# Kernel tuning notes

Measured on AMD Instinct MI355X. Metric: run time of the kernel, lower is better.

The kernel has to match this reference:

```python
import jax, jax.numpy as jnp
import numpy as np

K = 16
EPS = 1e-5  # BatchNorm eps (torch default)


def _lin(t, w, b):
    # 1x1 Conv2d over channel dim == per-point linear
    return jnp.einsum('bnkc,cd->bnkd', t, w) + b


def _bn(t, g, b):
    # BatchNorm2d (training-mode batch stats) over all dims except channels
    m = jnp.mean(t, axis=(0, 1, 2), keepdims=True)
    v = jnp.var(t, axis=(0, 1, 2), keepdims=True)
    return (t - m) * jax.lax.rsqrt(v + EPS) * g + b


def setup_inputs() -> dict:
    key = jax.random.key(0)
    ks = jax.random.split(key, 8)
    B, N, C, OUT = 4, 4096, 61, 128
    IN = C + 3  # 64 = in_feat_dim

    def w(k, i, o):
        return jax.random.normal(k, (i, o), jnp.float32) * (1.0 / np.sqrt(i))

    return {
        'x': jax.random.normal(ks[0], (B, N, C), jnp.float32),
        'pos': jax.random.uniform(ks[1], (B, N, 3), jnp.float32),
        # relation_vec_to_weights_net: 10 -> 32 -> IN -> IN (no BN, last_act=False)
        'rw1': w(ks[2], 10, 32), 'rb1': jnp.zeros((32,), jnp.float32),
        'rw2': w(ks[3], 32, IN), 'rb2': jnp.zeros((IN,), jnp.float32),
        'rw3': w(ks[4], IN, IN), 'rb3': jnp.zeros((IN,), jnp.float32),
        # feat_mlp_net: IN -> OUT -> OUT (BN, last_act=False)
        'fw1': w(ks[5], IN, OUT), 'fb1': jnp.zeros((OUT,), jnp.float32),
        'g1': jnp.ones((OUT,), jnp.float32), 'b1': jnp.zeros((OUT,), jnp.float32),
        'fw2': w(ks[6], OUT, OUT), 'fb2': jnp.zeros((OUT,), jnp.float32),
        'g2': jnp.ones((OUT,), jnp.float32), 'b2': jnp.zeros((OUT,), jnp.float32),
    }


def reference(x, pos, rw1, rb1, rw2, rb2, rw3, rb3,
              fw1, fb1, g1, b1, fw2, fb2, g2, b2):
    B, N, _ = x.shape
    # pairwise squared distances (B,N,N); sampled_idx=None -> all points are centers
    d2 = jnp.sum((pos[:, :, None, :] - pos[:, None, :, :]) ** 2, axis=-1)
    _, idx = jax.lax.top_k(-d2, K)                      # kNN indices (B,N,K)
    gather = jax.vmap(lambda v, i: v[i])                # per-batch fancy gather
    gpos = gather(pos, idx)                             # (B,N,K,3)
    gx = gather(x, idx)                                 # (B,N,K,C)
    cpos = pos[:, :, None, :]                           # center positions (B,N,1,3)
    rel = gpos - cpos                                   # relative pos (B,N,K,3)
    s = jnp.sum(rel ** 2, axis=-1, keepdims=True)
    # safe L2 norm (grad 0 at 0, like torch.norm)
    dis = jnp.where(s > 0, jnp.sqrt(jnp.where(s > 0, s, 1.0)), 0.0)
    relation = jnp.concatenate(
        [jnp.broadcast_to(cpos, gpos.shape), gpos, rel, dis], axis=-1)  # (B,N,K,10)
    h = jax.nn.relu(_lin(relation, rw1, rb1))
    h = jax.nn.relu(_lin(h, rw2, rb2))
    weights = _lin(h, rw3, rb3)                         # (B,N,K,IN), no last act
    feat = jnp.concatenate([gx, gpos], axis=-1)         # (B,N,K,IN)
    feat = weights * feat
    feat = jnp.max(feat, axis=2, keepdims=True)         # max-pool over K -> (B,N,1,IN)
    feat = jax.nn.relu(feat)
    feat = jax.nn.relu(_bn(_lin(feat, fw1, fb1), g1, b1))
    feat = _bn(_lin(feat, fw2, fb2), g2, b2)            # last_act=False
    return feat[:, :, 0, :]                             # (B,N,OUT)
```

## Files before the change

kernel.cpp:

```cpp
#include <hip/hip_runtime.h>
#include <hip/hip_bf16.h>
#include <math.h>

#define NPTS   4096
#define NB     4
#define NC     61
#define NK     16
#define NROWS  16384
#define BN_EPS 1e-5f
#define INV_ROWS (1.0f/16384.0f)

#define GRD    8
#define NCELL  512
#define CELLH  0.125f

__global__ __launch_bounds__(256) void prep_kernel(const float* __restrict__ pos,
                                                   float4* __restrict__ pos4,
                                                   int* __restrict__ cellOf,
                                                   int* __restrict__ counts) {
    const int i = blockIdx.x * 256 + threadIdx.x;
    if (i >= NB * NPTS) return;
    const float px = pos[i * 3 + 0], py = pos[i * 3 + 1], pz = pos[i * 3 + 2];
    pos4[i] = make_float4(px, py, pz, 0.f);
    const int cx = min(GRD - 1, max(0, (int)(px * GRD)));
    const int cy = min(GRD - 1, max(0, (int)(py * GRD)));
    const int cz = min(GRD - 1, max(0, (int)(pz * GRD)));
    const int cid = ((cz << 3) + cy) * GRD + cx;
    cellOf[i] = cid;
    atomicAdd(&counts[(i >> 12) * NCELL + cid], 1);
}

__global__ __launch_bounds__(512) void scan_kernel(const int* __restrict__ counts,
                                                   int* __restrict__ cellStart) {
    __shared__ int s[NCELL];
    const int b = blockIdx.x, t = threadIdx.x;
    s[t] = counts[b * NCELL + t];
    __syncthreads();
    for (int off = 1; off < NCELL; off <<= 1) {
        const int v = (t >= off) ? s[t - off] : 0;
        __syncthreads();
        s[t] += v;
        __syncthreads();
    }
    cellStart[b * (NCELL + 1) + t + 1] = s[t];
    if (t == 0) cellStart[b * (NCELL + 1)] = 0;
}

__global__ __launch_bounds__(256) void scatter_kernel(const float4* __restrict__ pos4,
                                                      const int* __restrict__ cellOf,
                                                      const int* __restrict__ cellStart,
                                                      int* __restrict__ fill,
                                                      float4* __restrict__ spt) {
    const int i = blockIdx.x * 256 + threadIdx.x;
    if (i >= NB * NPTS) return;
    const int b = i >> 12;
    const int cid = cellOf[i];
    const int dst = cellStart[b * (NCELL + 1) + cid] + atomicAdd(&fill[b * NCELL + cid], 1);
    float4 p = pos4[i];
    p.w = __int_as_float(i & 4095);
    spt[(b << 12) + dst] = p;
}

#define OCAP 8
#define NPAD 257

__global__ __launch_bounds__(256) void knn_kernel(const float4* __restrict__ pos4,
                                                  const float4* __restrict__ spt,
                                                  const int* __restrict__ cellStart,
                                                  int* __restrict__ idx_out,
                                                  int* __restrict__ flagcnt,
                                                  int* __restrict__ flaglist) {
    __shared__ unsigned long long buf[OCAP * NPAD];
    const int t  = threadIdx.x;
    const int l8 = t & 7;
    const int q  = blockIdx.x * 32 + (t >> 3);
    const int b  = q >> 12;
    const float4* __restrict__ sb = spt + (b << 12);
    const int* __restrict__ cs = cellStart + b * (NCELL + 1);

    const float4 qp = pos4[q];
    const float qx = qp.x, qy = qp.y, qz = qp.z;
    const int cx = min(GRD - 1, max(0, (int)(qx * GRD)));
    const int cy = min(GRD - 1, max(0, (int)(qy * GRD)));
    const int cz = min(GRD - 1, max(0, (int)(qz * GRD)));
    const int x0 = max(0, cx - 1), x1 = min(GRD - 1, cx + 1);

    unsigned long long bk[16];
#pragma unroll
    for (int i = 0; i < 16; ++i) bk[i] = ~0ull;
    unsigned int thr_bits = 0xFFFFFFFFu;
    int owptr = 0;

    auto compact = [&]() {
        unsigned long long od[OCAP];
#pragma unroll
        for (int s = 0; s < OCAP; ++s) {
            const unsigned long long v = buf[s * NPAD + t];
            od[s] = (s < owptr) ? v : ~0ull;
        }
        owptr = 0;
#pragma unroll
        for (int k = 2; k <= 8; k <<= 1) {
#pragma unroll
            for (int j = k >> 1; j > 0; j >>= 1) {
#pragma unroll
                for (int i = 0; i < 8; ++i) {
                    const int l = i ^ j;
                    if (l > i) {
                        const bool up = ((i & k) == 0);
                        const unsigned long long a = od[i], c = od[l];
                        const bool sw = up ? (c < a) : (a < c);
                        od[i] = sw ? c : a;
                        od[l] = sw ? a : c;
                    }
                }
            }
        }
#pragma unroll
        for (int i = 8; i < 16; ++i) {
            const unsigned long long c = od[15 - i];
            bk[i] = (c < bk[i]) ? c : bk[i];
        }
#pragma unroll
        for (int j = 8; j > 0; j >>= 1) {
#pragma unroll
            for (int i = 0; i < 16; ++i) {
                const int l = i ^ j;
                if (l > i) {
                    const unsigned long long a = bk[i], c = bk[l];
                    const bool sw = (c < a);
                    bk[i] = sw ? c : a;
                    bk[l] = sw ? a : c;
                }
            }
        }
        unsigned int th = (unsigned int)(bk[15] >> 32);
#pragma unroll
        for (int m = 1; m <= 4; m <<= 1) {
            const unsigned int o = __shfl_xor(th, m, 8);
            th = (o < th) ? o : th;
        }
        thr_bits = th;
    };

    for (int rz = 0; rz < 3; ++rz) {
        for (int ry = 0; ry < 3; ++ry) {
            const int zz = cz + rz - 1, yy = cy + ry - 1;
            int rs = 0, re = 0;
            if (zz >= 0 && zz < GRD && yy >= 0 && yy < GRD) {
                const int rowb = ((zz << 3) + yy) << 3;
                rs = cs[rowb + x0];
                re = cs[rowb + x1 + 1];
            }
            int p = rs + l8;
            while (__any(p < re)) {
                if (p < re) {
                    const float4 c = sb[p];
                    const float dx = qx - c.x, dy = qy - c.y, dz = qz - c.z;
                    const float d2 = __fadd_rn(__fadd_rn(__fmul_rn(dx, dx), __fmul_rn(dy, dy)),
                                               __fmul_rn(dz, dz));
                    if (__float_as_uint(d2) < thr_bits) {
                        buf[owptr * NPAD + t] =
                            ((unsigned long long)__float_as_uint(d2) << 32) |
                            (unsigned int)__float_as_int(c.w);
                        owptr++;
                    }
                }
                p += 8;
                if (__any(owptr >= OCAP - 1)) compact();
            }
        }
    }
    compact();

#pragma unroll
    for (int m = 1; m <= 4; m <<= 1) {
        unsigned long long ot[16];
#pragma unroll
        for (int i = 0; i < 16; ++i) ot[i] = __shfl_xor(bk[i], m, 8);
#pragma unroll
        for (int i = 0; i < 16; ++i) {
            const unsigned long long c = ot[15 - i];
            bk[i] = (c < bk[i]) ? c : bk[i];
        }
#pragma unroll
        for (int j = 8; j > 0; j >>= 1) {
#pragma unroll
            for (int i = 0; i < 16; ++i) {
                const int l = i ^ j;
                if (l > i) {
                    const unsigned long long a = bk[i], c = bk[l];
                    const bool sw = (c < a);
                    bk[i] = sw ? c : a;
                    bk[l] = sw ? a : c;
                }
            }
        }
    }

    if (l8 == 0) {
        const int ob = q * NK;
        *(int4*)&idx_out[ob + 0]  = make_int4((int)bk[0],  (int)bk[1],  (int)bk[2],  (int)bk[3]);
        *(int4*)&idx_out[ob + 4]  = make_int4((int)bk[4],  (int)bk[5],  (int)bk[6],  (int)bk[7]);
        *(int4*)&idx_out[ob + 8]  = make_int4((int)bk[8],  (int)bk[9],  (int)bk[10], (int)bk[11]);
        *(int4*)&idx_out[ob + 12] = make_int4((int)bk[12], (int)bk[13], (int)bk[14], (int)bk[15]);

        const int y0 = max(0, cy - 1), y1 = min(GRD - 1, cy + 1);
        const int z0 = max(0, cz - 1), z1 = min(GRD - 1, cz + 1);
        float mg = 1e30f;
        if (x0 > 0)       mg = fminf(mg, qx - x0 * CELLH);
        if (x1 < GRD - 1) mg = fminf(mg, (x1 + 1) * CELLH - qx);
        if (y0 > 0)       mg = fminf(mg, qy - y0 * CELLH);
        if (y1 < GRD - 1) mg = fminf(mg, (y1 + 1) * CELLH - qy);
        if (z0 > 0)       mg = fminf(mg, qz - z0 * CELLH);
        if (z1 < GRD - 1) mg = fminf(mg, (z1 + 1) * CELLH - qz);
        mg = fmaxf(mg - 1e-5f, 0.f);
        const float mg2 = mg * mg;
        if ((unsigned int)(bk[15] >> 32) >= __float_as_uint(mg2)) {
            const int slot = atomicAdd(flagcnt, 1);
            flaglist[slot] = q;
        }
    }
}

__global__ __launch_bounds__(256) void knn_fallback(const float4* __restrict__ pos4,
                                                    int* __restrict__ idx_out,
                                                    const int* __restrict__ flagcnt,
                                                    const int* __restrict__ flaglist) {
    __shared__ unsigned long long wres[4 * 16];
    const int nf = flagcnt[0];
    const int t = threadIdx.x;
    const int w = t >> 6;

    for (int fi = blockIdx.x; fi < nf; fi += 64) {
        const int qi = flaglist[fi];
        const int b = qi >> 12;
        const float4* __restrict__ pb = pos4 + (b << 12);
        const float4 qp = pb[qi & 4095];

        float4 c[16];
#pragma unroll
        for (int s = 0; s < 16; ++s) c[s] = pb[(s << 8) | t];

        unsigned long long key[16];
#pragma unroll
        for (int s = 0; s < 16; ++s) {
            const int j = (s << 8) | t;
            const float dx = qp.x - c[s].x, dy = qp.y - c[s].y, dz = qp.z - c[s].z;
            const float d2 = __fadd_rn(__fadd_rn(__fmul_rn(dx, dx), __fmul_rn(dy, dy)),
                                       __fmul_rn(dz, dz));
            key[s] = ((unsigned long long)__float_as_uint(d2) << 32) | (unsigned int)j;
        }

#pragma unroll
        for (int k = 2; k <= 16; k <<= 1) {
#pragma unroll
            for (int j = k >> 1; j > 0; j >>= 1) {
#pragma unroll
                for (int i = 0; i < 16; ++i) {
                    const int l = i ^ j;
                    if (l > i) {
                        const bool up = ((i & k) == 0);
                        const unsigned long long a = key[i], cc = key[l];
                        const bool sw = up ? (cc < a) : (a < cc);
                        key[i] = sw ? cc : a;
                        key[l] = sw ? a : cc;
                    }
                }
            }
        }

#pragma unroll
        for (int m = 1; m <= 32; m <<= 1) {
            unsigned long long ot[16];
#pragma unroll
            for (int i = 0; i < 16; ++i) ot[i] = __shfl_xor(key[i], m, 64);
#pragma unroll
            for (int i = 0; i < 16; ++i) {
                const unsigned long long cc = ot[15 - i];
                key[i] = (cc < key[i]) ? cc : key[i];
            }
#pragma unroll
            for (int j = 8; j > 0; j >>= 1) {
#pragma unroll
                for (int i = 0; i < 16; ++i) {
                    const int l = i ^ j;
                    if (l > i) {
                        const unsigned long long a = key[i], cc = key[l];
                        const bool sw = (cc < a);
                        key[i] = sw ? cc : a;
                        key[l] = sw ? a : cc;
                    }
                }
            }
        }

        if ((t & 63) == 0) {
#pragma unroll
            for (int i = 0; i < 16; ++i) wres[w * 16 + i] = key[i];
        }
        __syncthreads();

        if (t == 0) {
            int hp[4] = {0, 0, 0, 0};
            const int ob = qi * NK;
            for (int o = 0; o < NK; ++o) {
                unsigned long long bestk = ~0ull;
                int bestw = 0;
#pragma unroll
                for (int w2 = 0; w2 < 4; ++w2) {
                    const unsigned long long h = (hp[w2] < 16) ? wres[w2 * 16 + hp[w2]] : ~0ull;
                    if (h < bestk) { bestk = h; bestw = w2; }
                }
                idx_out[ob + o] = (int)(bestk & 0xFFFFFFFFu);
                hp[bestw]++;
            }
        }
        __syncthreads();
    }
}

__device__ __forceinline__ unsigned int f2bf(float f) {
    unsigned int b = __float_as_uint(f);
    return (b + 0x7FFFu + ((b >> 16) & 1u)) >> 16;
}
#define BFLO(u) __uint_as_float((u) << 16)
#define BFHI(u) __uint_as_float((u) & 0xFFFF0000u)

__global__ __launch_bounds__(256) void mlp_kernel(
    const float4* __restrict__ pos4, const float* __restrict__ x,
    const int* __restrict__ idx,
    const float* __restrict__ rw1, const float* __restrict__ rb1,
    const float* __restrict__ rw2, const float* __restrict__ rb2,
    const float* __restrict__ rw3, const float* __restrict__ rb3,
    float* __restrict__ pooled) {
    __shared__ float w1s[320], b1s[32], b2s[64], b3s[64];
    __shared__ unsigned int w2p[1024];
    __shared__ unsigned int w3p[2048];
    const int t = threadIdx.x;
    for (int i = t; i < 320; i += 256)  w1s[i] = rw1[i];
    for (int i = t; i < 1024; i += 256) {
        const int row = i >> 5, q = i & 31;
        w2p[i] = f2bf(rw2[row * 64 + 2 * q]) | (f2bf(rw2[row * 64 + 2 * q + 1]) << 16);
    }
    for (int i = t; i < 2048; i += 256) {
        const int o = i >> 5, q = i & 31;
        w3p[i] = f2bf(rw3[(2 * q) * 64 + o]) | (f2bf(rw3[(2 * q + 1) * 64 + o]) << 16);
    }
    if (t < 32)                 b1s[t] = rb1[t];
    else if (t >= 32 && t < 96) b2s[t - 32] = rb2[t - 32];
    else if (t >= 96 && t < 160) b3s[t - 96] = rb3[t - 96];
    __syncthreads();

    const int k8   = t & 7;
    const int qloc = t >> 3;
    const int q    = blockIdx.x * 32 + qloc;
    const int b    = q >> 12, n = q & 4095;
    const int j0 = idx[(size_t)q * NK + k8];
    const int j1 = idx[(size_t)q * NK + k8 + 8];
    const float4* __restrict__ pb = pos4 + (b << 12);

    const float4 cp = pb[n];
    const float4 pa = pb[j0];
    const float4 pc = pb[j1];
    const float rxa = pa.x - cp.x, rya = pa.y - cp.y, rza = pa.z - cp.z;
    const float rxb = pc.x - cp.x, ryb = pc.y - cp.y, rzb = pc.z - cp.z;
    const float ssa = rxa * rxa + rya * rya + rza * rza;
    const float ssb = rxb * rxb + ryb * ryb + rzb * rzb;
    const float disa = (ssa > 0.f) ? sqrtf(ssa) : 0.f;
    const float disb = (ssb > 0.f) ? sqrtf(ssb) : 0.f;
    const float rina[10] = {cp.x, cp.y, cp.z, pa.x, pa.y, pa.z, rxa, rya, rza, disa};
    const float rinb[10] = {cp.x, cp.y, cp.z, pc.x, pc.y, pc.z, rxb, ryb, rzb, disb};

    float h1a[32], h1b[32];
#pragma unroll
    for (int o = 0; o < 32; ++o) { h1a[o] = b1s[o]; h1b[o] = h1a[o]; }
#pragma unroll
    for (int i = 0; i < 10; ++i) {
        const float va = rina[i], vb = rinb[i];
#pragma unroll
        for (int o = 0; o < 32; ++o) {
            const float w = w1s[i * 32 + o];
            h1a[o] += va * w; h1b[o] += vb * w;
        }
    }
#pragma unroll
    for (int o = 0; o < 32; ++o) { h1a[o] = fmaxf(h1a[o], 0.f); h1b[o] = fmaxf(h1b[o], 0.f); }

    float h2a[64], h2b[64];
#pragma unroll
    for (int o = 0; o < 64; ++o) { h2a[o] = b2s[o]; h2b[o] = h2a[o]; }
    for (int i = 0; i < 32; ++i) {
        const float va = h1a[i], vb = h1b[i];
#pragma unroll
        for (int op = 0; op < 8; ++op) {
            const uint4 u = *(const uint4*)&w2p[(i << 5) + (op << 2)];
            const int o = op << 3;
            const float w0 = BFLO(u.x), w1 = BFHI(u.x), w2 = BFLO(u.y), w3 = BFHI(u.y);
            const float w4 = BFLO(u.z), w5 = BFHI(u.z), w6 = BFLO(u.w), w7 = BFHI(u.w);
            h2a[o+0] += va*w0; h2b[o+0] += vb*w0;
            h2a[o+1] += va*w1; h2b[o+1] += vb*w1;
            h2a[o+2] += va*w2; h2b[o+2] += vb*w2;
            h2a[o+3] += va*w3; h2b[o+3] += vb*w3;
            h2a[o+4] += va*w4; h2b[o+4] += vb*w4;
            h2a[o+5] += va*w5; h2b[o+5] += vb*w5;
            h2a[o+6] += va*w6; h2b[o+6] += vb*w6;
            h2a[o+7] += va*w7; h2b[o+7] += vb*w7;
        }
    }
#pragma unroll
    for (int o = 0; o < 64; ++o) { h2a[o] = fmaxf(h2a[o], 0.f); h2b[o] = fmaxf(h2b[o], 0.f); }

    const float* __restrict__ xr0 = x + (size_t)((b << 12) | j0) * NC;
    const float* __restrict__ xr1 = x + (size_t)((b << 12) | j1) * NC;
    float* __restrict__ pout = pooled + (size_t)q * 64;

    for (int o = 0; o < 64; ++o) {
        float acca = b3s[o], accb = acca;
#pragma unroll
        for (int ip = 0; ip < 8; ++ip) {
            const uint4 u = *(const uint4*)&w3p[(o << 5) + (ip << 2)];
            const int i = ip << 3;
            const float w0 = BFLO(u.x), w1 = BFHI(u.x), w2 = BFLO(u.y), w3 = BFHI(u.y);
            const float w4 = BFLO(u.z), w5 = BFHI(u.z), w6 = BFLO(u.w), w7 = BFHI(u.w);
            acca += h2a[i+0]*w0 + h2a[i+1]*w1 + h2a[i+2]*w2 + h2a[i+3]*w3
                  + h2a[i+4]*w4 + h2a[i+5]*w5 + h2a[i+6]*w6 + h2a[i+7]*w7;
            accb += h2b[i+0]*w0 + h2b[i+1]*w1 + h2b[i+2]*w2 + h2b[i+3]*w3
                  + h2b[i+4]*w4 + h2b[i+5]*w5 + h2b[i+6]*w6 + h2b[i+7]*w7;
        }
        const float fa = (o < NC) ? xr0[o] : (o == 61 ? pa.x : (o == 62 ? pa.y : pa.z));
        const float fb = (o < NC) ? xr1[o] : (o == 61 ? pc.x : (o == 62 ? pc.y : pc.z));
        float f = fmaxf(fa * acca, fb * accb);
#pragma unroll
        for (int m = 1; m < 8; m <<= 1) f = fmaxf(f, __shfl_xor(f, m, 8));
        if (k8 == 0) pout[o] = fmaxf(f, 0.f);
    }
}

__global__ __launch_bounds__(256) void gemm1_kernel(
    const float* __restrict__ A, const float* __restrict__ W,
    const float* __restrict__ bias, float* __restrict__ y,
    float* __restrict__ sum, float* __restrict__ sumsq) {
    __shared__ float As[64 * 64];
    __shared__ float Bs[64 * 128];
    const int t = threadIdx.x;
    const int r0 = blockIdx.x * 64;
    for (int i = t; i < 64 * 128; i += 256) Bs[i] = W[i];
    for (int i = t; i < 64 * 64; i += 256)  As[i] = A[(size_t)r0 * 64 + i];
    __syncthreads();

    const int c = t & 127, rg = t >> 7;
    float acc[32];
    const float bv = bias[c];
#pragma unroll
    for (int r = 0; r < 32; ++r) acc[r] = bv;

    for (int kk = 0; kk < 64; kk += 4) {
        const float b0 = Bs[(kk + 0) * 128 + c];
        const float b1 = Bs[(kk + 1) * 128 + c];
        const float b2 = Bs[(kk + 2) * 128 + c];
        const float b3 = Bs[(kk + 3) * 128 + c];
#pragma unroll
        for (int r = 0; r < 32; ++r) {
            const float4 a = *(const float4*)&As[(rg * 32 + r) * 64 + kk];
            acc[r] += a.x * b0 + a.y * b1 + a.z * b2 + a.w * b3;
        }
    }

    float s = 0.f, s2 = 0.f;
#pragma unroll
    for (int r = 0; r < 32; ++r) {
        const float v = acc[r];
        s += v; s2 += v * v;
        y[(size_t)(r0 + rg * 32 + r) * 128 + c] = v;
    }
    __syncthreads();
    As[t] = s; As[256 + t] = s2;
    __syncthreads();
    if (rg == 0) {
        atomicAdd(&sum[c],   As[c] + As[128 + c]);
        atomicAdd(&sumsq[c], As[256 + c] + As[256 + 128 + c]);
    }
}

__global__ __launch_bounds__(256) void gemm2_kernel(
    const float* __restrict__ y1, const float* __restrict__ W,
    const float* __restrict__ bias,
    const float* __restrict__ sum1, const float* __restrict__ sumsq1,
    const float* __restrict__ g1, const float* __restrict__ b1,
    float* __restrict__ y2, float* __restrict__ sum2, float* __restrict__ sumsq2) {
    __shared__ float As[64 * 128];
    __shared__ float Bs[64 * 128];
    __shared__ float a1s[128], s1s[128];
    const int t = threadIdx.x;
    const int r0 = blockIdx.x * 64;

    if (t < 128) {
        const float m = sum1[t] * INV_ROWS;
        const float v = sumsq1[t] * INV_ROWS - m * m;
        const float a = rsqrtf(v + BN_EPS) * g1[t];
        a1s[t] = a; s1s[t] = b1[t] - m * a;
    }
    for (int i = t; i < 64 * 128; i += 256) Bs[i] = W[i];
    __syncthreads();
    for (int i = t; i < 64 * 128; i += 256) {
        const int cc = i & 127;
        const float v = y1[(size_t)r0 * 128 + i];
        As[i] = fmaxf(v * a1s[cc] + s1s[cc], 0.f);
    }
    __syncthreads();

    const int c = t & 127, rg = t >> 7;
    float acc[32];
    const float bv = bias[c];
#pragma unroll
    for (int r = 0; r < 32; ++r) acc[r] = bv;

    for (int kk = 0; kk < 64; kk += 4) {
        const float b0 = Bs[(kk + 0) * 128 + c];
        const float b1v = Bs[(kk + 1) * 128 + c];
        const float b2 = Bs[(kk + 2) * 128 + c];
        const float b3 = Bs[(kk + 3) * 128 + c];
#pragma unroll
        for (int r = 0; r < 32; ++r) {
            const float4 a = *(const float4*)&As[(rg * 32 + r) * 128 + kk];
            acc[r] += a.x * b0 + a.y * b1v + a.z * b2 + a.w * b3;
        }
    }
    __syncthreads();
    for (int i = t; i < 64 * 128; i += 256) Bs[i] = W[64 * 128 + i];
    __syncthreads();
    for (int kk = 0; kk < 64; kk += 4) {
        const float b0 = Bs[(kk + 0) * 128 + c];
        const float b1v = Bs[(kk + 1) * 128 + c];
        const float b2 = Bs[(kk + 2) * 128 + c];
        const float b3 = Bs[(kk + 3) * 128 + c];
#pragma unroll
        for (int r = 0; r < 32; ++r) {
            const float4 a = *(const float4*)&As[(rg * 32 + r) * 128 + 64 + kk];
            acc[r] += a.x * b0 + a.y * b1v + a.z * b2 + a.w * b3;
        }
    }

    float s = 0.f, s2 = 0.f;
#pragma unroll
    for (int r = 0; r < 32; ++r) {
        const float v = acc[r];
        s += v; s2 += v * v;
        y2[(size_t)(r0 + rg * 32 + r) * 128 + c] = v;
    }
    __syncthreads();
    As[t] = s; As[256 + t] = s2;
    __syncthreads();
    if (rg == 0) {
        atomicAdd(&sum2[c],   As[c] + As[128 + c]);
        atomicAdd(&sumsq2[c], As[256 + c] + As[256 + 128 + c]);
    }
}

__global__ __launch_bounds__(256) void bnout_kernel(
    const float* __restrict__ y2, const float* __restrict__ sum2,
    const float* __restrict__ sumsq2, const float* __restrict__ g2,
    const float* __restrict__ b2, float* __restrict__ out) {
    const int i = blockIdx.x * 256 + threadIdx.x;
    const int c = i & 127;
    const float m = sum2[c] * INV_ROWS;
    const float v = sumsq2[c] * INV_ROWS - m * m;
    const float a = rsqrtf(v + BN_EPS) * g2[c];
    out[i] = y2[i] * a + (b2[c] - m * a);
}

extern "C" void kernel_launch(void* const* d_in, const int* in_sizes, int n_in,
                              void* d_out, int out_size, void* d_ws, size_t ws_size,
                              hipStream_t stream) {
    const float* x   = (const float*)d_in[0];
    const float* pos = (const float*)d_in[1];
    const float* rw1 = (const float*)d_in[2];
    const float* rb1 = (const float*)d_in[3];
    const float* rw2 = (const float*)d_in[4];
    const float* rb2 = (const float*)d_in[5];
    const float* rw3 = (const float*)d_in[6];
    const float* rb3 = (const float*)d_in[7];
    const float* fw1 = (const float*)d_in[8];
    const float* fb1 = (const float*)d_in[9];
    const float* g1  = (const float*)d_in[10];
    const float* b1  = (const float*)d_in[11];
    const float* fw2 = (const float*)d_in[12];
    const float* fb2 = (const float*)d_in[13];
    const float* g2  = (const float*)d_in[14];
    const float* b2  = (const float*)d_in[15];
    float* out = (float*)d_out;

    char* ws = (char*)d_ws;
    int*    idx      = (int*)ws;
    float*  pooled   = (float*)(ws + (1u << 20));
    float*  y1       = (float*)(ws + (5u << 20));
    float*  y2       = (float*)(ws + (13u << 20));
    float*  stats    = (float*)(ws + (21u << 20));
    float*  sum1 = stats, *sumsq1 = stats + 128, *sum2 = stats + 256, *sumsq2 = stats + 384;
    int*    counts   = (int*)(stats + 512);
    int*    fill     = counts + NB * NCELL;
    int*    flagcnt  = fill + NB * NCELL;
    int*    cellStart= (int*)(ws + (21u << 20) + (20u << 10));
    int*    cellOf   = (int*)(ws + (21u << 20) + (32u << 10));
    int*    flaglist = (int*)(ws + (21u << 20) + (96u << 10));
    float4* pos4     = (float4*)(ws + (22u << 20));
    float4* spt      = (float4*)(ws + (22u << 20) + (256u << 10));

    hipMemsetAsync(stats, 0, (512 + 2048 + 2048 + 1) * sizeof(float), stream);

    prep_kernel<<<64, 256, 0, stream>>>(pos, pos4, cellOf, counts);
    scan_kernel<<<NB, 512, 0, stream>>>(counts, cellStart);
    scatter_kernel<<<64, 256, 0, stream>>>(pos4, cellOf, cellStart, fill, spt);
    knn_kernel<<<512, 256, 0, stream>>>(pos4, spt, cellStart, idx, flagcnt, flaglist);
    knn_fallback<<<64, 256, 0, stream>>>(pos4, idx, flagcnt, flaglist);
    mlp_kernel<<<512, 256, 0, stream>>>(pos4, x, idx, rw1, rb1, rw2, rb2, rw3, rb3, pooled);
    gemm1_kernel<<<256, 256, 0, stream>>>(pooled, fw1, fb1, y1, sum1, sumsq1);
    gemm2_kernel<<<256, 256, 0, stream>>>(y1, fw2, fb2, sum1, sumsq1, g1, b1, y2, sum2, sumsq2);
    bnout_kernel<<<NROWS * 128 / 256, 256, 0, stream>>>(y2, sum2, sumsq2, g2, b2, out);
}
```

Baseline: 320.7 us.

## Rewrite relation-weight MLP with bf16 MFMA tiles per wavefront

The per-neighbor 3-layer relation MLP moves from scalar FMAs over register arrays to MFMA 16x16x32 bf16 matrix instructions. Each wavefront handles 64 (point, neighbor) rows and stages intermediate activations through LDS scratch as bf16. The layer-1 bias is folded in as a constant-one input column, and the grid doubles to 1024 blocks. This is meant to cut the large FP32 ALU cost and register pressure of the MLP, at the price of bf16 rounding of inputs and activations, LDS round-trips, and scattered gathers of x in the epilogue.

```diff
diff --git a/kernel.cpp b/kernel.cpp
--- a/kernel.cpp
+++ b/kernel.cpp
@@ -13,6 +13,9 @@
 #define GRD    8
 #define NCELL  512
 #define CELLH  0.125f
+
+typedef short bf16x8 __attribute__((ext_vector_type(8)));
+typedef float f32x4  __attribute__((ext_vector_type(4)));
 
 __global__ __launch_bounds__(256) void prep_kernel(const float* __restrict__ pos,
                                                    float4* __restrict__ pos4,
@@ -324,8 +327,6 @@
     unsigned int b = __float_as_uint(f);
     return (b + 0x7FFFu + ((b >> 16) & 1u)) >> 16;
 }
-#define BFLO(u) __uint_as_float((u) << 16)
-#define BFHI(u) __uint_as_float((u) & 0xFFFF0000u)
 
 __global__ __launch_bounds__(256) void mlp_kernel(
     const float4* __restrict__ pos4, const float* __restrict__ x,
@@ -334,106 +335,160 @@
     const float* __restrict__ rw2, const float* __restrict__ rb2,
     const float* __restrict__ rw3, const float* __restrict__ rb3,
     float* __restrict__ pooled) {
-    __shared__ float w1s[320], b1s[32], b2s[64], b3s[64];
-    __shared__ unsigned int w2p[1024];
-    __shared__ unsigned int w3p[2048];
+    __shared__ __attribute__((aligned(16))) unsigned short w1t[32 * 40];
+    __shared__ __attribute__((aligned(16))) unsigned short w2t[64 * 40];
+    __shared__ __attribute__((aligned(16))) unsigned short w3t[64 * 72];
+    __shared__ __attribute__((aligned(16))) unsigned short scr[4 * 64 * 72];
+
     const int t = threadIdx.x;
-    for (int i = t; i < 320; i += 256)  w1s[i] = rw1[i];
-    for (int i = t; i < 1024; i += 256) {
-        const int row = i >> 5, q = i & 31;
-        w2p[i] = f2bf(rw2[row * 64 + 2 * q]) | (f2bf(rw2[row * 64 + 2 * q + 1]) << 16);
-    }
-    for (int i = t; i < 2048; i += 256) {
-        const int o = i >> 5, q = i & 31;
-        w3p[i] = f2bf(rw3[(2 * q) * 64 + o]) | (f2bf(rw3[(2 * q + 1) * 64 + o]) << 16);
-    }
-    if (t < 32)                 b1s[t] = rb1[t];
-    else if (t >= 32 && t < 96) b2s[t - 32] = rb2[t - 32];
-    else if (t >= 96 && t < 160) b3s[t - 96] = rb3[t - 96];
-    __syncthreads();
-
-    const int k8   = t & 7;
-    const int qloc = t >> 3;
-    const int q    = blockIdx.x * 32 + qloc;
-    const int b    = q >> 12, n = q & 4095;
-    const int j0 = idx[(size_t)q * NK + k8];
-    const int j1 = idx[(size_t)q * NK + k8 + 8];
-    const float4* __restrict__ pb = pos4 + (b << 12);
-
-    const float4 cp = pb[n];
-    const float4 pa = pb[j0];
-    const float4 pc = pb[j1];
-    const float rxa = pa.x - cp.x, rya = pa.y - cp.y, rza = pa.z - cp.z;
-    const float rxb = pc.x - cp.x, ryb = pc.y - cp.y, rzb = pc.z - cp.z;
-    const float ssa = rxa * rxa + rya * rya + rza * rza;
-    const float ssb = rxb * rxb + ryb * ryb + rzb * rzb;
-    const float disa = (ssa > 0.f) ? sqrtf(ssa) : 0.f;
-    const float disb = (ssb > 0.f) ? sqrtf(ssb) : 0.f;
-    const float rina[10] = {cp.x, cp.y, cp.z, pa.x, pa.y, pa.z, rxa, rya, rza, disa};
-    const float rinb[10] = {cp.x, cp.y, cp.z, pc.x, pc.y, pc.z, rxb, ryb, rzb, disb};
-
-    float h1a[32], h1b[32];
-#pragma unroll
-    for (int o = 0; o < 32; ++o) { h1a[o] = b1s[o]; h1b[o] = h1a[o]; }
-#pragma unroll
-    for (int i = 0; i < 10; ++i) {
-        const float va = rina[i], vb = rinb[i];
-#pragma unroll
-        for (int o = 0; o < 32; ++o) {
-            const float w = w1s[i * 32 + o];
-            h1a[o] += va * w; h1b[o] += vb * w;
-        }
-    }
-#pragma unroll
-    for (int o = 0; o < 32; ++o) { h1a[o] = fmaxf(h1a[o], 0.f); h1b[o] = fmaxf(h1b[o], 0.f); }
-
-    float h2a[64], h2b[64];
-#pragma unroll
-    for (int o = 0; o < 64; ++o) { h2a[o] = b2s[o]; h2b[o] = h2a[o]; }
-    for (int i = 0; i < 32; ++i) {
-        const float va = h1a[i], vb = h1b[i];
-#pragma unroll
-        for (int op = 0; op < 8; ++op) {
-            const uint4 u = *(const uint4*)&w2p[(i << 5) + (op << 2)];
-            const int o = op << 3;
-            const float w0 = BFLO(u.x), w1 = BFHI(u.x), w2 = BFLO(u.y), w3 = BFHI(u.y);
-            const float w4 = BFLO(u.z), w5 = BFHI(u.z), w6 = BFLO(u.w), w7 = BFHI(u.w);
-            h2a[o+0] += va*w0; h2b[o+0] += vb*w0;
-            h2a[o+1] += va*w1; h2b[o+1] += vb*w1;
-            h2a[o+2] += va*w2; h2b[o+2] += vb*w2;
-            h2a[o+3] += va*w3; h2b[o+3] += vb*w3;
-            h2a[o+4] += va*w4; h2b[o+4] += vb*w4;
-            h2a[o+5] += va*w5; h2b[o+5] += vb*w5;
-            h2a[o+6] += va*w6; h2b[o+6] += vb*w6;
-            h2a[o+7] += va*w7; h2b[o+7] += vb*w7;
-        }
-    }
-#pragma unroll
-    for (int o = 0; o < 64; ++o) { h2a[o] = fmaxf(h2a[o], 0.f); h2b[o] = fmaxf(h2b[o], 0.f); }
-
-    const float* __restrict__ xr0 = x + (size_t)((b << 12) | j0) * NC;
-    const float* __restrict__ xr1 = x + (size_t)((b << 12) | j1) * NC;
-    float* __restrict__ pout = pooled + (size_t)q * 64;
-
-    for (int o = 0; o < 64; ++o) {
-        float acca = b3s[o], accb = acca;
-#pragma unroll
-        for (int ip = 0; ip < 8; ++ip) {
-            const uint4 u = *(const uint4*)&w3p[(o << 5) + (ip << 2)];
-            const int i = ip << 3;
-            const float w0 = BFLO(u.x), w1 = BFHI(u.x), w2 = BFLO(u.y), w3 = BFHI(u.y);
-            const float w4 = BFLO(u.z), w5 = BFHI(u.z), w6 = BFLO(u.w), w7 = BFHI(u.w);
-            acca += h2a[i+0]*w0 + h2a[i+1]*w1 + h2a[i+2]*w2 + h2a[i+3]*w3
-                  + h2a[i+4]*w4 + h2a[i+5]*w5 + h2a[i+6]*w6 + h2a[i+7]*w7;
-            accb += h2b[i+0]*w0 + h2b[i+1]*w1 + h2b[i+2]*w2 + h2b[i+3]*w3
-                  + h2b[i+4]*w4 + h2b[i+5]*w5 + h2b[i+6]*w6 + h2b[i+7]*w7;
-        }
-        const float fa = (o < NC) ? xr0[o] : (o == 61 ? pa.x : (o == 62 ? pa.y : pa.z));
-        const float fb = (o < NC) ? xr1[o] : (o == 61 ? pc.x : (o == 62 ? pc.y : pc.z));
-        float f = fmaxf(fa * acca, fb * accb);
-#pragma unroll
-        for (int m = 1; m < 8; m <<= 1) f = fmaxf(f, __shfl_xor(f, m, 8));
-        if (k8 == 0) pout[o] = fmaxf(f, 0.f);
+    for (int i = t; i < 32 * 32; i += 256) {
+        const int n = i >> 5, k = i & 31;
+        float v = 0.f;
+        if (k < 10) v = rw1[k * 32 + n];
+        else if (k == 15) v = rb1[n];
+        w1t[n * 40 + k] = (unsigned short)f2bf(v);
+    }
+    for (int i = t; i < 64 * 32; i += 256) {
+        const int n = i >> 5, k = i & 31;
+        w2t[n * 40 + k] = (unsigned short)f2bf(rw2[k * 64 + n]);
+    }
+    for (int i = t; i < 64 * 64; i += 256) {
+        const int n = i >> 6, k = i & 63;
+        w3t[n * 72 + k] = (unsigned short)f2bf(rw3[k * 64 + n]);
+    }
+    __syncthreads();
+
+    const int lane = t & 63;
+    const int quad = lane >> 4;
+    const int l16  = lane & 15;
+    unsigned short* __restrict__ ws = &scr[(t >> 6) * 64 * 72];
+
+    const int rowbase = blockIdx.x * 256 + (t & 192);
+    const int b = rowbase >> 16;
+    const float4* __restrict__ pb = pos4 + ((size_t)b << 12);
+    const float* __restrict__ xb = x + ((size_t)b << 12) * NC;
+
+    {
+        const int row_g = rowbase + lane;
+        const int q = row_g >> 4;
+        const int j = idx[row_g];
+        const float4 cp = pb[q & 4095];
+        const float4 gp = pb[j];
+        const float rx = gp.x - cp.x, ry = gp.y - cp.y, rz = gp.z - cp.z;
+        const float ss = rx * rx + ry * ry + rz * rz;
+        const float dis = (ss > 0.f) ? sqrtf(ss) : 0.f;
+        unsigned int d[20];
+#pragma unroll
+        for (int i = 0; i < 20; ++i) d[i] = 0;
+        d[0] = f2bf(cp.x) | (f2bf(cp.y) << 16);
+        d[1] = f2bf(cp.z) | (f2bf(gp.x) << 16);
+        d[2] = f2bf(gp.y) | (f2bf(gp.z) << 16);
+        d[3] = f2bf(rx)   | (f2bf(ry) << 16);
+        d[4] = f2bf(rz)   | (f2bf(dis) << 16);
+        d[7] = 0x3F800000u;
+        unsigned int* wr = (unsigned int*)&ws[lane * 40];
+#pragma unroll
+        for (int i = 0; i < 20; ++i) wr[i] = d[i];
+    }
+    __builtin_amdgcn_s_waitcnt(0);
+
+    const f32x4 zero = {0.f, 0.f, 0.f, 0.f};
+
+    bf16x8 a1[4], b1f[2];
+#pragma unroll
+    for (int mt = 0; mt < 4; ++mt)
+        a1[mt] = *(const bf16x8*)&ws[(mt * 16 + l16) * 40 + quad * 8];
+#pragma unroll
+    for (int nt = 0; nt < 2; ++nt)
+        b1f[nt] = *(const bf16x8*)&w1t[(nt * 16 + l16) * 40 + quad * 8];
+
+    f32x4 c1[2][4];
+#pragma unroll
+    for (int nt = 0; nt < 2; ++nt)
+#pragma unroll
+        for (int mt = 0; mt < 4; ++mt)
+            c1[nt][mt] = __builtin_amdgcn_mfma_f32_16x16x32_bf16(a1[mt], b1f[nt], zero, 0, 0, 0);
+
+#pragma unroll
+    for (int nt = 0; nt < 2; ++nt)
+#pragma unroll
+        for (int mt = 0; mt < 4; ++mt)
+#pragma unroll
+            for (int r = 0; r < 4; ++r)
+                ws[(mt * 16 + quad * 4 + r) * 40 + nt * 16 + l16] =
+                    (unsigned short)f2bf(fmaxf(c1[nt][mt][r], 0.f));
+    __builtin_amdgcn_s_waitcnt(0);
+
+    float b2v[4], b3v[4];
+#pragma unroll
+    for (int nt = 0; nt < 4; ++nt) { b2v[nt] = rb2[nt * 16 + l16]; b3v[nt] = rb3[nt * 16 + l16]; }
+
+    bf16x8 a2[4];
+#pragma unroll
+    for (int mt = 0; mt < 4; ++mt)
+        a2[mt] = *(const bf16x8*)&ws[(mt * 16 + l16) * 40 + quad * 8];
+
+    f32x4 c2[4][4];
+#pragma unroll
+    for (int nt = 0; nt < 4; ++nt) {
+        const bf16x8 b2f = *(const bf16x8*)&w2t[(nt * 16 + l16) * 40 + quad * 8];
+#pragma unroll
+        for (int mt = 0; mt < 4; ++mt)
+            c2[nt][mt] = __builtin_amdgcn_mfma_f32_16x16x32_bf16(a2[mt], b2f, zero, 0, 0, 0);
+    }
+
+#pragma unroll
+    for (int nt = 0; nt < 4; ++nt)
+#pragma unroll
+        for (int mt = 0; mt < 4; ++mt)
+#pragma unroll
+            for (int r = 0; r < 4; ++r)
+                ws[(mt * 16 + quad * 4 + r) * 72 + nt * 16 + l16] =
+                    (unsigned short)f2bf(fmaxf(c2[nt][mt][r] + b2v[nt], 0.f));
+    __builtin_amdgcn_s_waitcnt(0);
+
+    bf16x8 a3[4][2];
+#pragma unroll
+    for (int mt = 0; mt < 4; ++mt)
+#pragma unroll
+        for (int kt = 0; kt < 2; ++kt)
+            a3[mt][kt] = *(const bf16x8*)&ws[(mt * 16 + l16) * 72 + kt * 32 + quad * 8];
+
+    f32x4 c3[4][4];
+#pragma unroll
+    for (int nt = 0; nt < 4; ++nt) {
+        const bf16x8 b3f0 = *(const bf16x8*)&w3t[(nt * 16 + l16) * 72 + 0 * 32 + quad * 8];
+        const bf16x8 b3f1 = *(const bf16x8*)&w3t[(nt * 16 + l16) * 72 + 1 * 32 + quad * 8];
+#pragma unroll
+        for (int mt = 0; mt < 4; ++mt) {
+            f32x4 acc = __builtin_amdgcn_mfma_f32_16x16x32_bf16(a3[mt][0], b3f0, zero, 0, 0, 0);
+            c3[nt][mt] = __builtin_amdgcn_mfma_f32_16x16x32_bf16(a3[mt][1], b3f1, acc, 0, 0, 0);
+        }
+    }
+
+#pragma unroll
+    for (int mt = 0; mt < 4; ++mt) {
+        const int qg = (rowbase >> 4) + mt;
+        int jrow[4];
+#pragma unroll
+        for (int r = 0; r < 4; ++r) jrow[r] = idx[rowbase + mt * 16 + quad * 4 + r];
+#pragma unroll
+        for (int nt = 0; nt < 4; ++nt) {
+            const int col = nt * 16 + l16;
+            float mx = -1e30f;
+#pragma unroll
+            for (int r = 0; r < 4; ++r) {
+                const int j = jrow[r];
+                float fv;
+                if (col < NC) fv = xb[(size_t)j * NC + col];
+                else          fv = ((const float*)&pb[j])[col - NC];
+                mx = fmaxf(mx, fv * (c3[nt][mt][r] + b3v[nt]));
+            }
+            mx = fmaxf(mx, __shfl_xor(mx, 16, 64));
+            mx = fmaxf(mx, __shfl_xor(mx, 32, 64));
+            mx = fmaxf(mx, 0.f);
+            if (quad == 0) pooled[(size_t)qg * 64 + col] = mx;
+        }
     }
 }
 
@@ -614,7 +669,7 @@
     scatter_kernel<<<64, 256, 0, stream>>>(pos4, cellOf, cellStart, fill, spt);
     knn_kernel<<<512, 256, 0, stream>>>(pos4, spt, cellStart, idx, flagcnt, flaglist);
     knn_fallback<<<64, 256, 0, stream>>>(pos4, idx, flagcnt, flaglist);
-    mlp_kernel<<<512, 256, 0, stream>>>(pos4, x, idx, rw1, rb1, rw2, rb2, rw3, rb3, pooled);
+    mlp_kernel<<<1024, 256, 0, stream>>>(pos4, x, idx, rw1, rb1, rw2, rb2, rw3, rb3, pooled);
     gemm1_kernel<<<256, 256, 0, stream>>>(pooled, fw1, fb1, y1, sum1, sumsq1);
     gemm2_kernel<<<256, 256, 0, stream>>>(y1, fw2, fb2, sum1, sumsq1, g1, b1, y2, sum2, sumsq2);
     bnout_kernel<<<NROWS * 128 / 256, 256, 0, stream>>>(y2, sum2, sumsq2, g2, b2, out);
```

Measured after the change: 260.7 us. 1.23x faster.
